# Performance work log

Hardware: AMD Instinct MI355X
Metric: run time of the kernel (lower is better)

The kernel has to match this reference:

```python
import jax, jax.numpy as jnp
import numpy as np
import math

B, S, E, H = 2, 2048, 1024, 16
D = E // H  # head_size = 64
EPS = 1e-5

def _ln(x, g, b):
    mu = jnp.mean(x, axis=-1, keepdims=True)
    var = jnp.mean(jnp.square(x - mu), axis=-1, keepdims=True)
    return (x - mu) * jax.lax.rsqrt(var + EPS) * g + b

def setup_inputs() -> dict:
    key = jax.random.key(0)
    ks = jax.random.split(key, 16)
    s = 0.02
    return {
        "I": jax.random.normal(ks[0], (B, S, E), jnp.float32),
        "x": jax.random.normal(ks[1], (B, S, E), jnp.float32),
        "mask": jnp.ones((B, 1, S), jnp.int32),
        # per-head Q/K/V weights stacked over heads [H, E, D], biases [H, D]
        "wq": jax.random.normal(ks[2], (H, E, D), jnp.float32) * s,
        "bq": jax.random.normal(ks[3], (H, D), jnp.float32) * s,
        "wk": jax.random.normal(ks[4], (H, E, D), jnp.float32) * s,
        "bk": jax.random.normal(ks[5], (H, D), jnp.float32) * s,
        "wv": jax.random.normal(ks[6], (H, E, D), jnp.float32) * s,
        "bv": jax.random.normal(ks[7], (H, D), jnp.float32) * s,
        "w_proj": jax.random.normal(ks[8], (E, E), jnp.float32) * s,
        "b_proj": jnp.zeros((E,), jnp.float32),
        "g1": jnp.ones((E,), jnp.float32),
        "be1": jnp.zeros((E,), jnp.float32),
        "g2": jnp.ones((E,), jnp.float32),
        "be2": jnp.zeros((E,), jnp.float32),
        "w1": jax.random.normal(ks[9], (E, 4 * E), jnp.float32) * s,
        "b1": jnp.zeros((4 * E,), jnp.float32),
        "w2": jax.random.normal(ks[10], (4 * E, E), jnp.float32) * s,
        "b2": jnp.zeros((E,), jnp.float32),
    }

def reference(I, x, mask, wq, bq, wk, bk, wv, bv, w_proj, b_proj,
              g1, be1, g2, be2, w1, b1, w2, b2):
    xn = _ln(x, g1, be1)
    # batched per-head projections: [B,S,E] x [H,E,D] -> [B,H,S,D]
    q = jnp.einsum('bse,hed->bhsd', I, wq) + bq[None, :, None, :]
    k = jnp.einsum('bse,hed->bhsd', xn, wk) + bk[None, :, None, :]
    v = jnp.einsum('bse,hed->bhsd', xn, wv) + bv[None, :, None, :]
    # NOTE: original scales by sqrt(n_embed), not sqrt(head_size)
    scores = jnp.einsum('bhqd,bhkd->bhqk', q, k) / math.sqrt(E)
    scores = jnp.where(mask[:, None, :, :] == 0, -1e9, scores)
    attn = jax.nn.softmax(scores, axis=-1)
    ctx = jnp.einsum('bhqk,bhkd->bhqd', attn, v)
    # concat heads: [B,S,H,D] -> [B,S,E]
    ctx = ctx.transpose(0, 2, 1, 3).reshape(B, S, E)
    attn_out = ctx @ w_proj + b_proj
    h = xn + attn_out
    h2 = _ln(h, g2, be2)
    ff = jax.nn.gelu(h2 @ w1 + b1, approximate=False) @ w2 + b2
    return h2 + ff
```

## Files before the change

kernel.cpp:

```cpp
#include <hip/hip_runtime.h>
#include <hip/hip_bf16.h>
#include <math.h>

typedef short short8 __attribute__((ext_vector_type(8)));
typedef short short4_t __attribute__((ext_vector_type(4)));
typedef float f32x4 __attribute__((ext_vector_type(4)));
typedef unsigned short u16;
typedef unsigned int u32;

#define B_ 2
#define S_ 2048
#define E_ 1024
#define H_ 16
#define D_ 64
#define TOK (B_*S_)

__device__ __forceinline__ float bf2f(u16 u) {
    union { unsigned int u; float f; } v; v.u = ((unsigned int)u) << 16; return v.f;
}
__device__ __forceinline__ u16 f2bf(float f) {
    union { float f; unsigned int u; } v; v.f = f;
    unsigned int r = v.u + 0x7fffu + ((v.u >> 16) & 1u);
    return (u16)(r >> 16);
}
__device__ __forceinline__ u32 fbits(float f) {
    union { float f; u32 u; } v; v.f = f; return v.u;
}
__device__ __forceinline__ void gl_lds16(const u16* g, short* l) {
    __builtin_amdgcn_global_load_lds(
        (const __attribute__((address_space(1))) unsigned int*)(g),
        (__attribute__((address_space(3))) unsigned int*)(l), 16, 0, 0);
}


__device__ __forceinline__ void convf_body(const float* __restrict__ s, u16* __restrict__ d,
                                           int blk, int tid)
{
    size_t i = ((size_t)blk * 256 + tid) * 8;
    f32x4 a = *(const f32x4*)(s + i);
    f32x4 b = *(const f32x4*)(s + i + 4);
    short8 r;
#pragma unroll
    for (int j = 0; j < 4; j++) { r[j] = (short)f2bf(a[j]); r[4 + j] = (short)f2bf(b[j]); }
    *(short8*)(d + i) = r;
}

__device__ __forceinline__ void tconv_body(const float* __restrict__ src, u16* __restrict__ dst,
                                           int K, int N, int bx, int by, u16 (*t)[72], int tid)
{
    int k0 = by * 64, n0 = bx * 64;
    int kr = tid >> 4, nc = (tid & 15) * 4;
#pragma unroll
    for (int i = 0; i < 4; i++) {
        f32x4 v = *(const f32x4*)(src + (size_t)(k0 + kr + i * 16) * N + n0 + nc);
#pragma unroll
        for (int j = 0; j < 4; j++) t[kr + i * 16][nc + j] = f2bf(v[j]);
    }
    __syncthreads();
    int nr = tid >> 2, kg = (tid & 3) * 16;
    short8 r0, r1;
#pragma unroll
    for (int j = 0; j < 8; j++) { r0[j] = (short)t[kg + j][nr]; r1[j] = (short)t[kg + 8 + j][nr]; }
    u16* dp = dst + (size_t)(n0 + nr) * K + k0 + kg;
    *(short8*)(dp) = r0;
    *(short8*)(dp + 8) = r1;
}

__device__ __forceinline__ void tconvqkv_body(const float* __restrict__ wq, const float* __restrict__ wk,
                                              const float* __restrict__ wv, u16* __restrict__ dst,
                                              int z, int yy, u16 (*t)[72], int tid)
{
    int w = z >> 4, hh = z & 15;
    const float* src = (w == 0 ? wq : (w == 1 ? wk : wv)) + (size_t)hh * E_ * D_;
    u16* d = dst + (size_t)w * E_ * E_ + (size_t)hh * D_ * E_;
    int k0 = yy * 64;
    int kr = tid >> 4, nc = (tid & 15) * 4;
#pragma unroll
    for (int i = 0; i < 4; i++) {
        f32x4 v = *(const f32x4*)(src + (size_t)(k0 + kr + i * 16) * D_ + nc);
#pragma unroll
        for (int j = 0; j < 4; j++) t[kr + i * 16][nc + j] = f2bf(v[j]);
    }
    __syncthreads();
    int nr = tid >> 2, kg = (tid & 3) * 16;
    short8 r0, r1;
#pragma unroll
    for (int j = 0; j < 8; j++) { r0[j] = (short)t[kg + j][nr]; r1[j] = (short)t[kg + 8 + j][nr]; }
    u16* dp = d + (size_t)nr * E_ + k0 + kg;
    *(short8*)(dp) = r0;
    *(short8*)(dp + 8) = r1;
}

__device__ __forceinline__ void maskprep_body(const int* __restrict__ mask, float* __restrict__ fb,
                                              int* __restrict__ ok, int b, int tid, unsigned char* fl)
{
    int base = tid * 8;
    unsigned all = 1;
#pragma unroll
    for (int j = 0; j < 8; j++) {
        int m = mask[b * S_ + base + j];
        fb[b * S_ + base + j] = m ? 0.f : -1e9f;
        all &= (m != 0) ? 1u : 0u;
    }
    fl[tid] = (unsigned char)all;
    __syncthreads();
    if (tid < 32) {
        unsigned a = 1;
#pragma unroll
        for (int j = 0; j < 8; j++) a &= fl[tid * 8 + j];
        ok[b * 32 + tid] = (int)a;
    }
}

template<int INF32>
__device__ __forceinline__ void ln_body(const void* __restrict__ xv, const float* __restrict__ g,
                                        const float* __restrict__ be, u16* __restrict__ y,
                                        int blk, int tid)
{
    int lane = tid & 63, wave = tid >> 6;
    int row = blk * 4 + wave;
    int c0 = lane * 16;
    float v[16];
    if (INF32) {
        const float* xr = (const float*)xv + (size_t)row * E_ + c0;
#pragma unroll
        for (int i = 0; i < 4; i++) {
            f32x4 xx = *(const f32x4*)(xr + i * 4);
#pragma unroll
            for (int j = 0; j < 4; j++) v[i * 4 + j] = xx[j];
        }
    } else {
        const u16* xr = (const u16*)xv + (size_t)row * E_ + c0;
        short8 a = *(const short8*)(xr);
        short8 b = *(const short8*)(xr + 8);
#pragma unroll
        for (int j = 0; j < 8; j++) { v[j] = bf2f((u16)a[j]); v[8 + j] = bf2f((u16)b[j]); }
    }
    float s = 0.f, q = 0.f;
#pragma unroll
    for (int i = 0; i < 16; i++) { s += v[i]; q += v[i] * v[i]; }
#pragma unroll
    for (int off = 1; off < 64; off <<= 1) {
        s += __shfl_xor(s, off, 64);
        q += __shfl_xor(q, off, 64);
    }
    float mu = s * (1.0f / E_);
    float var = q * (1.0f / E_) - mu * mu;
    float rstd = rsqrtf(var + 1e-5f);
    u16* yr = y + (size_t)row * E_ + c0;
    short8 o0, o1;
#pragma unroll
    for (int j = 0; j < 8; j++) {
        o0[j] = (short)f2bf((v[j] - mu) * rstd * g[c0 + j] + be[c0 + j]);
        o1[j] = (short)f2bf((v[8 + j] - mu) * rstd * g[c0 + 8 + j] + be[c0 + 8 + j]);
    }
    *(short8*)(yr) = o0;
    *(short8*)(yr + 8) = o1;
}

__global__ __launch_bounds__(256) void prep_k(
    const float* __restrict__ I, u16* __restrict__ Ibf,
    const float* __restrict__ wq, const float* __restrict__ wk,
    const float* __restrict__ wv, u16* __restrict__ WTqkv,
    const float* __restrict__ w_proj, u16* __restrict__ WTproj,
    const float* __restrict__ w1, u16* __restrict__ WT1,
    const float* __restrict__ w2, u16* __restrict__ WT2,
    const int* __restrict__ mask, float* __restrict__ fbm, int* __restrict__ okm,
    const float* __restrict__ x, const float* __restrict__ g1,
    const float* __restrict__ be1, u16* __restrict__ xn)
{
    __shared__ __align__(16) u16 tsh[64][72];
    int id = blockIdx.x, tid = threadIdx.x;
    if (id < 1024) {
        ln_body<1>(x, g1, be1, xn, id, tid);
    } else if (id < 3072) {
        convf_body(I, Ibf, id - 1024, tid);
    } else if (id < 3840) {
        int vb = id - 3072;
        tconvqkv_body(wq, wk, wv, WTqkv, vb >> 4, vb & 15, tsh, tid);
    } else if (id < 4096) {
        int vb = id - 3840;
        tconv_body(w_proj, WTproj, E_, E_, vb & 15, vb >> 4, tsh, tid);
    } else if (id < 5120) {
        int vb = id - 4096;
        tconv_body(w1, WT1, E_, 4 * E_, vb & 63, vb >> 6, tsh, tid);
    } else if (id < 6144) {
        int vb = id - 5120;
        tconv_body(w2, WT2, 4 * E_, E_, vb & 15, vb >> 4, tsh, tid);
    } else {
        maskprep_body(mask, fbm, okm, id - 6144, tid, (unsigned char*)tsh);
    }
}

__global__ __launch_bounds__(256) void vtrans_k(const u16* __restrict__ V, u16* __restrict__ Vt)
{
    __shared__ u16 t[64][72];
    int s0 = blockIdx.x * 64, h = blockIdx.y, b = blockIdx.z;
    int tid = threadIdx.x;
    int sr = tid >> 2, dc = (tid & 3) * 16;
    const u16* src = V + (size_t)b * S_ * E_ + (size_t)(s0 + sr) * E_ + h * D_ + dc;
    short8 v0 = *(const short8*)(src);
    short8 v1 = *(const short8*)(src + 8);
#pragma unroll
    for (int j = 0; j < 8; j++) { t[sr][dc + j] = v0[j]; t[sr][dc + 8 + j] = v1[j]; }
    __syncthreads();
    int dr = tid >> 2, sc = (tid & 3) * 16;
    short8 r0, r1;
#pragma unroll
    for (int j = 0; j < 8; j++) { r0[j] = (short)t[sc + j][dr]; r1[j] = (short)t[sc + 8 + j][dr]; }
    u16* dp = Vt + ((size_t)(b * H_ + h) * D_ + dr) * S_ + s0 + sc;
    *(short8*)(dp) = r0;
    *(short8*)(dp + 8) = r1;
}

template<int INF32>
__global__ __launch_bounds__(256) void ln_kernel(
    const void* __restrict__ xv, const float* __restrict__ g,
    const float* __restrict__ be, u16* __restrict__ y)
{
    ln_body<INF32>(xv, g, be, y, blockIdx.x, threadIdx.x);
}

template<int QKV, int GELU, int RX>
__global__ __launch_bounds__(512) void gemm8p_k(
    const u16* __restrict__ A, const u16* __restrict__ Axn,
    const u16* __restrict__ WT,
    const float* __restrict__ bq, const float* __restrict__ bk, const float* __restrict__ bv,
    u16* __restrict__ C, int M, int N, int K)
{
    __shared__ __align__(16) short As[2][256 * 64];
    __shared__ __align__(16) short Bs[2][256 * 64];
    int tid = threadIdx.x;
    int wave = tid >> 6, lane = tid & 63, quad = lane >> 4, l16 = lane & 15;
    int wm = wave >> 2, wn = wave & 3;

    int gx = gridDim.x, gy = gridDim.y;
    int lin = blockIdx.y * gx + blockIdx.x;
    int xcd = lin & 7, w = lin >> 3;
    int rw = gx / RX, rh = gy / (8 / RX);
    int bx = (xcd % RX) * rw + (w % rw);
    int by = (xcd / RX) * rh + (w / rw);
    int n0 = bx * 256, m0 = by * 256;

    int which = QKV ? (n0 >> 10) : 0;
    const u16* Ause = (QKV && which) ? Axn : A;
    const float* bias = QKV ? (which == 0 ? bq : (which == 1 ? bk : bv)) : bq;

    f32x4 acc[8][4];
#pragma unroll
    for (int m = 0; m < 8; m++)
#pragma unroll
        for (int n = 0; n < 4; n++)
            acc[m][n] = (f32x4){0.f, 0.f, 0.f, 0.f};

    int srow = lane >> 3, slot = lane & 7;
    const u16* Ag = Ause + (size_t)(m0 + wave * 16 + srow) * K + ((slot ^ srow) << 3);
    const u16* Bg = WT + (size_t)(n0 + wave * 16 + srow) * K + ((slot ^ srow) << 3);
    const size_t r8K = (size_t)8 * K, r128K = (size_t)128 * K, r136K = (size_t)136 * K;
    int wv = wave * 1024;
    int r7 = l16 & 7;
    int soff0 = (quad ^ r7) << 3;
    int soff1 = ((4 + quad) ^ r7) << 3;
    int arow = (wm * 128 + l16) * 64;
    int brow = (wn * 64 + l16) * 64;
    int NT = K >> 6;

#define SB __builtin_amdgcn_sched_barrier(0)
#define GLA2P(P, BUF, H) do { \
    gl_lds16((P) + ((H) ? r128K : (size_t)0), &As[BUF][wv + (H) * 8192]); \
    gl_lds16((P) + ((H) ? r136K : r8K), &As[BUF][wv + (H) * 8192 + 512]); } while (0)
#define GLB2P(P, BUF, H) do { \
    gl_lds16((P) + ((H) ? r128K : (size_t)0), &Bs[BUF][wv + (H) * 8192]); \
    gl_lds16((P) + ((H) ? r136K : r8K), &Bs[BUF][wv + (H) * 8192 + 512]); } while (0)
#define RDA(BUF, Mi, SO) (*(const short8*)(&As[BUF][arow + (Mi) * 1024 + (SO)]))
#define RDB(BUF, Ni, SO) (*(const short8*)(&Bs[BUF][brow + (Ni) * 1024 + (SO)]))
#define MM2(mb, R) do { \
    _Pragma("unroll") \
    for (int n_ = 0; n_ < 4; n_++) { \
        acc[(mb)][n_]     = __builtin_amdgcn_mfma_f32_16x16x32_bf16(R[0], bf[n_][0], acc[(mb)][n_], 0, 0, 0); \
        acc[(mb) + 1][n_] = __builtin_amdgcn_mfma_f32_16x16x32_bf16(R[1], bf[n_][0], acc[(mb) + 1][n_], 0, 0, 0); \
    } \
    _Pragma("unroll") \
    for (int n_ = 0; n_ < 4; n_++) { \
        acc[(mb)][n_]     = __builtin_amdgcn_mfma_f32_16x16x32_bf16(R[2], bf[n_][1], acc[(mb)][n_], 0, 0, 0); \
        acc[(mb) + 1][n_] = __builtin_amdgcn_mfma_f32_16x16x32_bf16(R[3], bf[n_][1], acc[(mb) + 1][n_], 0, 0, 0); \
    } \
} while (0)

#define KTILE(BUF, OBUF, TT, AO, BO) do { \
    SB; __builtin_amdgcn_s_barrier(); \
    short8 bf[4][2], af[4], ag[4]; \
    bf[0][0] = RDB(BUF, 0, soff0); bf[1][0] = RDB(BUF, 1, soff0); \
    bf[2][0] = RDB(BUF, 2, soff0); bf[3][0] = RDB(BUF, 3, soff0); \
    af[0] = RDA(BUF, 0, soff0); af[1] = RDA(BUF, 1, soff0); \
    bf[0][1] = RDB(BUF, 0, soff1); bf[1][1] = RDB(BUF, 1, soff1); \
    bf[2][1] = RDB(BUF, 2, soff1); bf[3][1] = RDB(BUF, 3, soff1); \
    af[2] = RDA(BUF, 0, soff1); af[3] = RDA(BUF, 1, soff1); \
    if ((TT) + 1 < NT) GLA2P((AO), OBUF, 0); \
    __builtin_amdgcn_s_setprio(1); MM2(0, af); __builtin_amdgcn_s_setprio(0); \
    ag[0] = RDA(BUF, 2, soff0); ag[1] = RDA(BUF, 3, soff0); \
    ag[2] = RDA(BUF, 2, soff1); ag[3] = RDA(BUF, 3, soff1); \
    SB; __builtin_amdgcn_s_barrier(); \
    if ((TT) + 1 < NT) GLA2P((AO), OBUF, 1); \
    __builtin_amdgcn_s_setprio(1); MM2(2, ag); __builtin_amdgcn_s_setprio(0); \
    af[0] = RDA(BUF, 4, soff0); af[1] = RDA(BUF, 5, soff0); \
    af[2] = RDA(BUF, 4, soff1); af[3] = RDA(BUF, 5, soff1); \
    SB; __builtin_amdgcn_s_barrier(); \
    if ((TT) + 2 < NT) GLB2P((BO), BUF, 0); \
    __builtin_amdgcn_s_setprio(1); MM2(4, af); __builtin_amdgcn_s_setprio(0); \
    ag[0] = RDA(BUF, 6, soff0); ag[1] = RDA(BUF, 7, soff0); \
    ag[2] = RDA(BUF, 6, soff1); ag[3] = RDA(BUF, 7, soff1); \
    SB; __builtin_amdgcn_s_barrier(); \
    if ((TT) + 2 < NT) GLB2P((BO), BUF, 1); \
    __builtin_amdgcn_s_setprio(1); MM2(6, ag); __builtin_amdgcn_s_setprio(0); \
    if ((TT) + 2 < NT) { asm volatile("s_waitcnt vmcnt(4)" ::: "memory"); } \
    else               { asm volatile("s_waitcnt vmcnt(0)" ::: "memory"); } \
    SB; \
} while (0)

    GLB2P(Bg, 0, 0); GLB2P(Bg, 0, 1);
    GLA2P(Ag, 0, 0); GLA2P(Ag, 0, 1);
    if (NT > 1) {
        GLB2P(Bg + 64, 1, 0); GLB2P(Bg + 64, 1, 1);
        asm volatile("s_waitcnt vmcnt(4)" ::: "memory");
    } else {
        asm volatile("s_waitcnt vmcnt(0)" ::: "memory");
    }

    const u16* A1 = Ag + 64;
    const u16* B2 = Bg + 128;
    for (int t = 0; t < NT; t += 2) {
        KTILE(0, 1, t, A1, B2);
        KTILE(1, 0, t + 1, A1 + 64, B2 + 64);
        A1 += 128; B2 += 128;
    }

    u16* Cw = QKV ? (C + (size_t)which * (size_t)M * 1024) : C;
    int ostride = QKV ? 1024 : N;
#pragma unroll
    for (int m = 0; m < 8; m++) {
#pragma unroll
        for (int n = 0; n < 4; n++) {
            int colg = n0 + wn * 64 + n * 16 + l16;
            int col = QKV ? (colg & 1023) : colg;
            float bb = bias[col];
#pragma unroll
            for (int r = 0; r < 4; r++) {
                int row = m0 + wm * 128 + m * 16 + quad * 4 + r;
                float v = acc[m][n][r] + bb;
                if (QKV && which == 0) v *= 0.03125f;
                if (GELU) v = 0.5f * v * (1.0f + erff(v * 0.70710678118f));
                Cw[(size_t)row * ostride + col] = f2bf(v);
            }
        }
    }
#undef SB
#undef GLA2P
#undef GLB2P
#undef RDA
#undef RDB
#undef MM2
#undef KTILE
}

__global__ __launch_bounds__(256) void gemmsk_k(
    const u16* __restrict__ A, const u16* __restrict__ WT,
    u16* __restrict__ P, int M, int N, int K, int Ks)
{
    __shared__ __align__(16) short a_sh[2][128 * 32];
    __shared__ __align__(16) short b_sh[2][128 * 32];
    int tid = threadIdx.x;
    int wave = tid >> 6, lane = tid & 63, quad = lane >> 4, l16 = lane & 15;
    int wm = wave >> 1, wn = wave & 1;
    int gx = gridDim.x;
    int lin = blockIdx.y * gx + blockIdx.x;
    int xcd = lin & 7, w = lin >> 3;
    int rh = gridDim.y >> 3;
    int bx = w % gx, by = xcd * rh + (w / gx);
    int m0 = by * 128, n0 = bx * 128;
    int koff = blockIdx.z * Ks;

    f32x4 acc[4][4];
#pragma unroll
    for (int mt = 0; mt < 4; mt++)
#pragma unroll
        for (int nt = 0; nt < 4; nt++)
            acc[mt][nt] = (f32x4){0.f, 0.f, 0.f, 0.f};

    int srow = lane >> 2;
    int c = ((lane & 3) ^ ((lane >> 3) & 3)) * 8;
    const u16* Ab = A + (size_t)(m0 + wave * 32 + srow) * K + koff + c;
    const u16* Bb = WT + (size_t)(n0 + wave * 32 + srow) * K + koff + c;
    short* al0 = &a_sh[0][wave * 1024];
    short* al1 = &a_sh[1][wave * 1024];
    short* bl0 = &b_sh[0][wave * 1024];
    short* bl1 = &b_sh[1][wave * 1024];
    int xo = (quad ^ ((l16 >> 1) & 3)) * 8;

    for (int kk = 0; kk < Ks; kk += 64) {
        __syncthreads();
        gl_lds16(Ab + kk, al0);
        gl_lds16(Ab + kk + (size_t)16 * K, al0 + 512);
        gl_lds16(Ab + kk + 32, al1);
        gl_lds16(Ab + kk + (size_t)16 * K + 32, al1 + 512);
        gl_lds16(Bb + kk, bl0);
        gl_lds16(Bb + kk + (size_t)16 * K, bl0 + 512);
        gl_lds16(Bb + kk + 32, bl1);
        gl_lds16(Bb + kk + (size_t)16 * K + 32, bl1 + 512);
        __syncthreads();

#pragma unroll
        for (int h = 0; h < 2; h++) {
            short8 af[4], bf8[4];
#pragma unroll
            for (int mt = 0; mt < 4; mt++)
                af[mt] = *(const short8*)(&a_sh[h][(wm * 64 + mt * 16 + l16) * 32 + xo]);
#pragma unroll
            for (int nt = 0; nt < 4; nt++)
                bf8[nt] = *(const short8*)(&b_sh[h][(wn * 64 + nt * 16 + l16) * 32 + xo]);
#pragma unroll
            for (int mt = 0; mt < 4; mt++)
#pragma unroll
                for (int nt = 0; nt < 4; nt++)
                    acc[mt][nt] = __builtin_amdgcn_mfma_f32_16x16x32_bf16(af[mt], bf8[nt], acc[mt][nt], 0, 0, 0);
        }
    }

    u16* Pz = P + (size_t)blockIdx.z * (size_t)M * N;
#pragma unroll
    for (int mt = 0; mt < 4; mt++) {
#pragma unroll
        for (int nt = 0; nt < 4; nt++) {
            int col = n0 + wn * 64 + nt * 16 + l16;
#pragma unroll
            for (int r = 0; r < 4; r++) {
                int row = m0 + wm * 64 + mt * 16 + quad * 4 + r;
                Pz[(size_t)row * N + col] = f2bf(acc[mt][nt][r]);
            }
        }
    }
}

__global__ __launch_bounds__(256) void combine2_k(
    const u16* __restrict__ P, const float* __restrict__ bias,
    const u16* __restrict__ res, float* __restrict__ out)
{
    const size_t MN = (size_t)TOK * E_;
    size_t i = ((size_t)blockIdx.x * 256 + threadIdx.x) * 8;
    int col = (int)(i & (E_ - 1));
    float v[8];
    f32x4 b0 = *(const f32x4*)(bias + col);
    f32x4 b1 = *(const f32x4*)(bias + col + 4);
    short8 rr = *(const short8*)(res + i);
#pragma unroll
    for (int j = 0; j < 4; j++) { v[j] = b0[j] + bf2f((u16)rr[j]); v[4 + j] = b1[j] + bf2f((u16)rr[4 + j]); }
#pragma unroll
    for (int z = 0; z < 2; z++) {
        short8 p = *(const short8*)(P + z * MN + i);
#pragma unroll
        for (int j = 0; j < 8; j++) v[j] += bf2f((u16)p[j]);
    }
    f32x4 o0, o1;
#pragma unroll
    for (int j = 0; j < 4; j++) { o0[j] = v[j]; o1[j] = v[4 + j]; }
    *(f32x4*)(out + i) = o0;
    *(f32x4*)(out + i + 4) = o1;
}

template<int GELU, int RES, int CF32>
__global__ __launch_bounds__(256) void gemm3_k(
    const u16* __restrict__ A, const u16* __restrict__ WT,
    const float* __restrict__ bias, const u16* __restrict__ res,
    void* __restrict__ Cv, int M, int N, int K)
{
    __shared__ __align__(16) short a_sh[2][128 * 32];
    __shared__ __align__(16) short b_sh[2][64 * 32];
    int tid = threadIdx.x;
    int wave = tid >> 6, lane = tid & 63, quad = lane >> 4, l16 = lane & 15;
    int wm = wave >> 1, wn = wave & 1;
    int m0 = blockIdx.y * 128, n0 = blockIdx.x * 64;

    f32x4 acc[4][2];
#pragma unroll
    for (int mt = 0; mt < 4; mt++)
#pragma unroll
        for (int nt = 0; nt < 2; nt++)
            acc[mt][nt] = (f32x4){0.f, 0.f, 0.f, 0.f};

    int srow = lane >> 2;
    int c = ((lane & 3) ^ ((lane >> 3) & 3)) * 8;
    const u16* Ab = A + (size_t)(m0 + wave * 32 + srow) * K + c;
    const u16* Bb = WT + (size_t)(n0 + wave * 16 + srow) * K + c;
    short* al0 = &a_sh[0][wave * 1024];
    short* al1 = &a_sh[1][wave * 1024];
    short* bl0 = &b_sh[0][wave * 512];
    short* bl1 = &b_sh[1][wave * 512];
    int xo = (quad ^ ((l16 >> 1) & 3)) * 8;

    for (int kk = 0; kk < K; kk += 64) {
        __syncthreads();
        gl_lds16(Ab + kk, al0);
        gl_lds16(Ab + kk + (size_t)16 * K, al0 + 512);
        gl_lds16(Ab + kk + 32, al1);
        gl_lds16(Ab + kk + (size_t)16 * K + 32, al1 + 512);
        gl_lds16(Bb + kk, bl0);
        gl_lds16(Bb + kk + 32, bl1);
        __syncthreads();

#pragma unroll
        for (int h = 0; h < 2; h++) {
            short8 af[4], bf8[2];
#pragma unroll
            for (int mt = 0; mt < 4; mt++)
                af[mt] = *(const short8*)(&a_sh[h][(wm * 64 + mt * 16 + l16) * 32 + xo]);
#pragma unroll
            for (int nt = 0; nt < 2; nt++)
                bf8[nt] = *(const short8*)(&b_sh[h][(wn * 32 + nt * 16 + l16) * 32 + xo]);
#pragma unroll
            for (int mt = 0; mt < 4; mt++)
#pragma unroll
                for (int nt = 0; nt < 2; nt++)
                    acc[mt][nt] = __builtin_amdgcn_mfma_f32_16x16x32_bf16(af[mt], bf8[nt], acc[mt][nt], 0, 0, 0);
        }
    }

#pragma unroll
    for (int mt = 0; mt < 4; mt++) {
#pragma unroll
        for (int nt = 0; nt < 2; nt++) {
            int col = n0 + wn * 32 + nt * 16 + l16;
            float bb = bias[col];
#pragma unroll
            for (int r = 0; r < 4; r++) {
                int row = m0 + wm * 64 + mt * 16 + quad * 4 + r;
                float v = acc[mt][nt][r] + bb;
                if (RES) v += bf2f(res[(size_t)row * N + col]);
                if (GELU) v = 0.5f * v * (1.0f + erff(v * 0.70710678118f));
                if (CF32) ((float*)Cv)[(size_t)row * N + col] = v;
                else ((u16*)Cv)[(size_t)row * N + col] = f2bf(v);
            }
        }
    }
}

__global__ __launch_bounds__(512) void attn_k(
    const u16* __restrict__ Q, const u16* __restrict__ K,
    const u16* __restrict__ Vt, const float* __restrict__ fb,
    const int* __restrict__ ok, u16* __restrict__ O)
{
    __shared__ __align__(16) short k_sh[2][2][64 * 32];
    __shared__ __align__(16) short v_sh[2][2][64 * 32];
    __shared__ __align__(16) short p_sh[8][16 * 72];
    int tid = threadIdx.x;
    int wave = tid >> 6, lane = tid & 63, quad = lane >> 4, l16 = lane & 15;
    int lin = blockIdx.x + 16 * (blockIdx.y + 16 * blockIdx.z);
    int xcd = lin & 7, w = lin >> 3;
    int combo = xcd * 4 + (w >> 4);
    int qb = w & 15, h = combo & 15, b = combo >> 4;
    int q0 = qb * 128;
    const u16* Qp = Q + (size_t)b * S_ * E_ + (size_t)h * D_;
    const u16* Kp = K + (size_t)b * S_ * E_ + (size_t)h * D_;
    const u16* Vtp = Vt + (size_t)(b * H_ + h) * D_ * S_;

    int qrow = q0 + wave * 16 + l16;
    short8 qf0 = *(const short8*)(Qp + (size_t)qrow * E_ + quad * 8);
    short8 qf1 = *(const short8*)(Qp + (size_t)qrow * E_ + 32 + quad * 8);

    f32x4 o[4];
#pragma unroll
    for (int dt = 0; dt < 4; dt++) o[dt] = (f32x4){0.f, 0.f, 0.f, 0.f};
    float rs_tot = 0.f;

    int sub = wave & 1, rblk = wave >> 1;
    int srow = lane >> 2;
    int c = ((lane & 3) ^ ((lane >> 3) & 3)) * 8;
    const u16* Kg = Kp + (size_t)(rblk * 16 + srow) * E_ + sub * 32 + c;
    const u16* Vg = Vtp + (size_t)(rblk * 16 + srow) * S_ + sub * 32 + c;
    short* kl0 = &k_sh[0][sub][rblk * 512];
    short* kl1 = &k_sh[1][sub][rblk * 512];
    short* vl0 = &v_sh[0][sub][rblk * 512];
    short* vl1 = &v_sh[1][sub][rblk * 512];

    gl_lds16(Kg, kl0);
    gl_lds16(Vg, vl0);
    __syncthreads();

    const float* fbb = fb + b * S_;
    const int* okb = ok + b * 32;
    int xo = (quad ^ ((l16 >> 1) & 3)) * 8;

    for (int kt = 0; kt < S_ / 64; kt++) {
        int cur = kt & 1;
        if (kt < 31) {
            gl_lds16(Kg + (size_t)(kt + 1) * 64 * E_, cur ? kl0 : kl1);
            gl_lds16(Vg + (kt + 1) * 64, cur ? vl0 : vl1);
        }

        f32x4 s[4];
#pragma unroll
        for (int mt = 0; mt < 4; mt++) {
            int ro = (mt * 16 + l16) * 32 + xo;
            short8 kf0 = *(const short8*)(&k_sh[cur][0][ro]);
            short8 kf1 = *(const short8*)(&k_sh[cur][1][ro]);
            s[mt] = __builtin_amdgcn_mfma_f32_16x16x32_bf16(kf0, qf0, (f32x4){0.f,0.f,0.f,0.f}, 0, 0, 0);
            s[mt] = __builtin_amdgcn_mfma_f32_16x16x32_bf16(kf1, qf1, s[mt], 0, 0, 0);
        }

        if (!okb[kt]) {
#pragma unroll
            for (int mt = 0; mt < 4; mt++)
#pragma unroll
                for (int r = 0; r < 4; r++)
                    s[mt][r] += fbb[kt * 64 + mt * 16 + quad * 4 + r];
        }

#pragma unroll
        for (int mt = 0; mt < 4; mt++) {
            float p0 = __expf(s[mt][0]);
            float p1 = __expf(s[mt][1]);
            float p2 = __expf(s[mt][2]);
            float p3 = __expf(s[mt][3]);
            rs_tot += (p0 + p1) + (p2 + p3);
            u32 u0 = __builtin_amdgcn_perm(fbits(p1), fbits(p0), 0x07060302u);
            u32 u1 = __builtin_amdgcn_perm(fbits(p3), fbits(p2), 0x07060302u);
            uint2 pk; pk.x = u0; pk.y = u1;
            *(uint2*)(&p_sh[wave][l16 * 72 + mt * 16 + quad * 4]) = pk;
        }

#pragma unroll
        for (int sk = 0; sk < 2; sk++) {
            short8 pf = *(const short8*)(&p_sh[wave][l16 * 72 + sk * 32 + quad * 8]);
#pragma unroll
            for (int dt = 0; dt < 4; dt++) {
                short8 vf = *(const short8*)(&v_sh[cur][sk][(dt * 16 + l16) * 32 + xo]);
                o[dt] = __builtin_amdgcn_mfma_f32_16x16x32_bf16(vf, pf, o[dt], 0, 0, 0);
            }
        }
        __syncthreads();
    }

    rs_tot += __shfl_xor(rs_tot, 16, 64);
    rs_tot += __shfl_xor(rs_tot, 32, 64);
    float inv = 1.0f / rs_tot;
    u16* Op = O + (size_t)b * S_ * E_ + (size_t)(q0 + wave * 16 + l16) * E_ + h * D_;
#pragma unroll
    for (int dt = 0; dt < 4; dt++) {
        short4_t pk;
#pragma unroll
        for (int r = 0; r < 4; r++) pk[r] = (short)f2bf(o[dt][r] * inv);
        *(short4_t*)(Op + dt * 16 + quad * 4) = pk;
    }
}

extern "C" void kernel_launch(void* const* d_in, const int* in_sizes, int n_in,
                              void* d_out, int out_size, void* d_ws, size_t ws_size,
                              hipStream_t stream)
{
    (void)in_sizes; (void)n_in; (void)out_size; (void)ws_size;
    const float* I      = (const float*)d_in[0];
    const float* x      = (const float*)d_in[1];
    const int*   mask   = (const int*)d_in[2];
    const float* wq     = (const float*)d_in[3];
    const float* bq     = (const float*)d_in[4];
    const float* wk     = (const float*)d_in[5];
    const float* bk     = (const float*)d_in[6];
    const float* wv     = (const float*)d_in[7];
    const float* bv     = (const float*)d_in[8];
    const float* w_proj = (const float*)d_in[9];
    const float* b_proj = (const float*)d_in[10];
    const float* g1     = (const float*)d_in[11];
    const float* be1    = (const float*)d_in[12];
    const float* g2     = (const float*)d_in[13];
    const float* be2    = (const float*)d_in[14];
    const float* w1     = (const float*)d_in[15];
    const float* b1     = (const float*)d_in[16];
    const float* w2     = (const float*)d_in[17];
    const float* b2     = (const float*)d_in[18];
    float* out = (float*)d_out;

    char* ws = (char*)d_ws;
    const size_t SZ = (size_t)TOK * E_;
    u16* xn   = (u16*)(ws);
    u16* qb_  = (u16*)(ws + SZ * 2);
    u16* kb_  = (u16*)(ws + SZ * 4);
    u16* vb_  = (u16*)(ws + SZ * 6);
    u16* Vt   = (u16*)(ws + SZ * 8);
    u16* Ibf  = (u16*)(ws + SZ * 8);
    u16* ctx  = (u16*)(ws + SZ * 6);
    u16* hb   = (u16*)(ws + SZ * 4);
    u16* h2   = (u16*)(ws);
    u16* a1   = (u16*)(ws + SZ * 2);
    u16* WTqkv  = (u16*)(ws + 40u * 1024 * 1024);
    u16* WTproj = (u16*)(ws + 46u * 1024 * 1024);
    u16* WT1    = (u16*)(ws + 48u * 1024 * 1024);
    u16* WT2    = (u16*)(ws + 56u * 1024 * 1024);
    u16* Pp     = (u16*)(ws + 40u * 1024 * 1024);
    float* fbm  = (float*)(ws + 40u * 1024 * 1024);
    int*   okm  = (int*)(ws + 40u * 1024 * 1024 + 16384);

    prep_k<<<dim3(6146), 256, 0, stream>>>(
        I, Ibf, wq, wk, wv, WTqkv, w_proj, WTproj, w1, WT1, w2, WT2,
        mask, fbm, okm, x, g1, be1, xn);

    gemm8p_k<1,0,2><<<dim3(12, TOK / 256), 512, 0, stream>>>(
        Ibf, xn, WTqkv, bq, bk, bv, qb_, TOK, 3072, E_);

    vtrans_k<<<dim3(S_ / 64, H_, B_), 256, 0, stream>>>(vb_, Vt);

    attn_k<<<dim3(S_ / 128, H_, B_), 512, 0, stream>>>(qb_, kb_, Vt, fbm, okm, ctx);

    gemm3_k<0,1,0><<<dim3(16, TOK / 128), 256, 0, stream>>>(
        ctx, WTproj, b_proj, xn, hb, TOK, E_, E_);
    ln_kernel<0><<<TOK / 4, 256, 0, stream>>>(hb, g2, be2, h2);
    gemm8p_k<0,1,2><<<dim3(16, TOK / 256), 512, 0, stream>>>(
        h2, nullptr, WT1, b1, nullptr, nullptr, a1, TOK, 4 * E_, E_);
    gemmsk_k<<<dim3(8, TOK / 128, 2), 256, 0, stream>>>(
        a1, WT2, Pp, TOK, E_, 4 * E_, 2 * E_);
    combine2_k<<<dim3(TOK * E_ / (256 * 8)), 256, 0, stream>>>(Pp, b2, h2, out);
}
```

Measured before the change: 361.0 us.

## Replace 256x256 K64 ping-pong GEMM with 128x256 K32 multi-block GEMM

Rewrites the QKV and FFN1 GEMM kernel to use 128x256 output tiles with a K-step of 32 and a much smaller LDS footprint. The launch bounds now request 4 blocks per CU so occupancy can hide latency, replacing the hand-scheduled ping-pong pipeline with its setprio and partial waitcnts. The grid doubles in the M direction, giving more blocks for better CU fill. The cost is less data reuse per tile, one full vmcnt(0) wait plus a barrier every K-step, and tighter register limits.

Measured after the change: 357.2 us. No clear change (-1.0%).

```diff
diff --git a/kernel.cpp b/kernel.cpp
--- a/kernel.cpp
+++ b/kernel.cpp
@@ -222,14 +222,14 @@
 }
 
 template<int QKV, int GELU, int RX>
-__global__ __launch_bounds__(512) void gemm8p_k(
+__global__ __launch_bounds__(512, 4) void gemmb32_k(
     const u16* __restrict__ A, const u16* __restrict__ Axn,
     const u16* __restrict__ WT,
     const float* __restrict__ bq, const float* __restrict__ bk, const float* __restrict__ bv,
     u16* __restrict__ C, int M, int N, int K)
 {
-    __shared__ __align__(16) short As[2][256 * 64];
-    __shared__ __align__(16) short Bs[2][256 * 64];
+    __shared__ __align__(16) short As[2][128 * 32];
+    __shared__ __align__(16) short Bs[2][256 * 32];
     int tid = threadIdx.x;
     int wave = tid >> 6, lane = tid & 63, quad = lane >> 4, l16 = lane & 15;
     int wm = wave >> 2, wn = wave & 3;
@@ -240,127 +240,81 @@
     int rw = gx / RX, rh = gy / (8 / RX);
     int bx = (xcd % RX) * rw + (w % rw);
     int by = (xcd / RX) * rh + (w / rw);
-    int n0 = bx * 256, m0 = by * 256;
+    int n0 = bx * 256, m0 = by * 128;
 
     int which = QKV ? (n0 >> 10) : 0;
     const u16* Ause = (QKV && which) ? Axn : A;
     const float* bias = QKV ? (which == 0 ? bq : (which == 1 ? bk : bv)) : bq;
 
-    f32x4 acc[8][4];
-#pragma unroll
-    for (int m = 0; m < 8; m++)
-#pragma unroll
-        for (int n = 0; n < 4; n++)
-            acc[m][n] = (f32x4){0.f, 0.f, 0.f, 0.f};
-
-    int srow = lane >> 3, slot = lane & 7;
-    const u16* Ag = Ause + (size_t)(m0 + wave * 16 + srow) * K + ((slot ^ srow) << 3);
-    const u16* Bg = WT + (size_t)(n0 + wave * 16 + srow) * K + ((slot ^ srow) << 3);
-    const size_t r8K = (size_t)8 * K, r128K = (size_t)128 * K, r136K = (size_t)136 * K;
-    int wv = wave * 1024;
-    int r7 = l16 & 7;
-    int soff0 = (quad ^ r7) << 3;
-    int soff1 = ((4 + quad) ^ r7) << 3;
-    int arow = (wm * 128 + l16) * 64;
-    int brow = (wn * 64 + l16) * 64;
-    int NT = K >> 6;
-
-#define SB __builtin_amdgcn_sched_barrier(0)
-#define GLA2P(P, BUF, H) do { \
-    gl_lds16((P) + ((H) ? r128K : (size_t)0), &As[BUF][wv + (H) * 8192]); \
-    gl_lds16((P) + ((H) ? r136K : r8K), &As[BUF][wv + (H) * 8192 + 512]); } while (0)
-#define GLB2P(P, BUF, H) do { \
-    gl_lds16((P) + ((H) ? r128K : (size_t)0), &Bs[BUF][wv + (H) * 8192]); \
-    gl_lds16((P) + ((H) ? r136K : r8K), &Bs[BUF][wv + (H) * 8192 + 512]); } while (0)
-#define RDA(BUF, Mi, SO) (*(const short8*)(&As[BUF][arow + (Mi) * 1024 + (SO)]))
-#define RDB(BUF, Ni, SO) (*(const short8*)(&Bs[BUF][brow + (Ni) * 1024 + (SO)]))
-#define MM2(mb, R) do { \
-    _Pragma("unroll") \
-    for (int n_ = 0; n_ < 4; n_++) { \
-        acc[(mb)][n_]     = __builtin_amdgcn_mfma_f32_16x16x32_bf16(R[0], bf[n_][0], acc[(mb)][n_], 0, 0, 0); \
-        acc[(mb) + 1][n_] = __builtin_amdgcn_mfma_f32_16x16x32_bf16(R[1], bf[n_][0], acc[(mb) + 1][n_], 0, 0, 0); \
-    } \
-    _Pragma("unroll") \
-    for (int n_ = 0; n_ < 4; n_++) { \
-        acc[(mb)][n_]     = __builtin_amdgcn_mfma_f32_16x16x32_bf16(R[2], bf[n_][1], acc[(mb)][n_], 0, 0, 0); \
-        acc[(mb) + 1][n_] = __builtin_amdgcn_mfma_f32_16x16x32_bf16(R[3], bf[n_][1], acc[(mb) + 1][n_], 0, 0, 0); \
-    } \
-} while (0)
-
-#define KTILE(BUF, OBUF, TT, AO, BO) do { \
-    SB; __builtin_amdgcn_s_barrier(); \
-    short8 bf[4][2], af[4], ag[4]; \
-    bf[0][0] = RDB(BUF, 0, soff0); bf[1][0] = RDB(BUF, 1, soff0); \
-    bf[2][0] = RDB(BUF, 2, soff0); bf[3][0] = RDB(BUF, 3, soff0); \
-    af[0] = RDA(BUF, 0, soff0); af[1] = RDA(BUF, 1, soff0); \
-    bf[0][1] = RDB(BUF, 0, soff1); bf[1][1] = RDB(BUF, 1, soff1); \
-    bf[2][1] = RDB(BUF, 2, soff1); bf[3][1] = RDB(BUF, 3, soff1); \
-    af[2] = RDA(BUF, 0, soff1); af[3] = RDA(BUF, 1, soff1); \
-    if ((TT) + 1 < NT) GLA2P((AO), OBUF, 0); \
-    __builtin_amdgcn_s_setprio(1); MM2(0, af); __builtin_amdgcn_s_setprio(0); \
-    ag[0] = RDA(BUF, 2, soff0); ag[1] = RDA(BUF, 3, soff0); \
-    ag[2] = RDA(BUF, 2, soff1); ag[3] = RDA(BUF, 3, soff1); \
-    SB; __builtin_amdgcn_s_barrier(); \
-    if ((TT) + 1 < NT) GLA2P((AO), OBUF, 1); \
-    __builtin_amdgcn_s_setprio(1); MM2(2, ag); __builtin_amdgcn_s_setprio(0); \
-    af[0] = RDA(BUF, 4, soff0); af[1] = RDA(BUF, 5, soff0); \
-    af[2] = RDA(BUF, 4, soff1); af[3] = RDA(BUF, 5, soff1); \
-    SB; __builtin_amdgcn_s_barrier(); \
-    if ((TT) + 2 < NT) GLB2P((BO), BUF, 0); \
-    __builtin_amdgcn_s_setprio(1); MM2(4, af); __builtin_amdgcn_s_setprio(0); \
-    ag[0] = RDA(BUF, 6, soff0); ag[1] = RDA(BUF, 7, soff0); \
-    ag[2] = RDA(BUF, 6, soff1); ag[3] = RDA(BUF, 7, soff1); \
-    SB; __builtin_amdgcn_s_barrier(); \
-    if ((TT) + 2 < NT) GLB2P((BO), BUF, 1); \
-    __builtin_amdgcn_s_setprio(1); MM2(6, ag); __builtin_amdgcn_s_setprio(0); \
-    if ((TT) + 2 < NT) { asm volatile("s_waitcnt vmcnt(4)" ::: "memory"); } \
-    else               { asm volatile("s_waitcnt vmcnt(0)" ::: "memory"); } \
-    SB; \
-} while (0)
-
-    GLB2P(Bg, 0, 0); GLB2P(Bg, 0, 1);
-    GLA2P(Ag, 0, 0); GLA2P(Ag, 0, 1);
-    if (NT > 1) {
-        GLB2P(Bg + 64, 1, 0); GLB2P(Bg + 64, 1, 1);
-        asm volatile("s_waitcnt vmcnt(4)" ::: "memory");
-    } else {
-        asm volatile("s_waitcnt vmcnt(0)" ::: "memory");
-    }
-
-    const u16* A1 = Ag + 64;
-    const u16* B2 = Bg + 128;
+    f32x4 acc[4][4];
+#pragma unroll
+    for (int mi = 0; mi < 4; mi++)
+#pragma unroll
+        for (int ni = 0; ni < 4; ni++)
+            acc[mi][ni] = (f32x4){0.f, 0.f, 0.f, 0.f};
+
+    int srow = lane >> 2, slot = lane & 3;
+    int kap = (srow >> 1) & 3;
+    const u16* Ag = Ause + (size_t)(m0 + wave * 16 + srow) * K + ((slot ^ kap) << 3);
+    const u16* Bg = WT + (size_t)(n0 + wave * 32 + srow) * K + ((slot ^ kap) << 3);
+    const size_t r16K = (size_t)16 * K;
+    int wA = wave * 512, wB = wave * 1024;
+    int so = (quad ^ ((l16 >> 1) & 3)) << 3;
+    int aoff = (wm * 64 + l16) * 32 + so;
+    int boff = (wn * 64 + l16) * 32 + so;
+    int NT = K >> 5;
+
+#define STAGEK(BUF, PA, PB) do { \
+    gl_lds16((PA), &As[BUF][wA]); \
+    gl_lds16((PB), &Bs[BUF][wB]); \
+    gl_lds16((PB) + r16K, &Bs[BUF][wB + 512]); } while (0)
+
+#define TILEK(BUF, OBUF, TT, PA, PB) do { \
+    if ((TT) + 1 < NT) STAGEK(OBUF, (PA), (PB)); \
+    short8 af[4], bf[4]; \
+    const short* ab = &As[BUF][aoff]; \
+    const short* bb = &Bs[BUF][boff]; \
+    _Pragma("unroll") for (int i_ = 0; i_ < 4; i_++) af[i_] = *(const short8*)(ab + i_ * 512); \
+    _Pragma("unroll") for (int i_ = 0; i_ < 4; i_++) bf[i_] = *(const short8*)(bb + i_ * 512); \
+    _Pragma("unroll") for (int mi = 0; mi < 4; mi++) \
+    _Pragma("unroll") for (int ni = 0; ni < 4; ni++) \
+        acc[mi][ni] = __builtin_amdgcn_mfma_f32_16x16x32_bf16(af[mi], bf[ni], acc[mi][ni], 0, 0, 0); \
+    asm volatile("s_waitcnt vmcnt(0)" ::: "memory"); \
+    __builtin_amdgcn_s_barrier(); } while (0)
+
+    STAGEK(0, Ag, Bg);
+    asm volatile("s_waitcnt vmcnt(0)" ::: "memory");
+    __builtin_amdgcn_s_barrier();
+
+    const u16* PA = Ag + 32;
+    const u16* PB = Bg + 32;
     for (int t = 0; t < NT; t += 2) {
-        KTILE(0, 1, t, A1, B2);
-        KTILE(1, 0, t + 1, A1 + 64, B2 + 64);
-        A1 += 128; B2 += 128;
+        TILEK(0, 1, t, PA, PB);
+        TILEK(1, 0, t + 1, PA + 32, PB + 32);
+        PA += 64; PB += 64;
     }
 
     u16* Cw = QKV ? (C + (size_t)which * (size_t)M * 1024) : C;
     int ostride = QKV ? 1024 : N;
 #pragma unroll
-    for (int m = 0; m < 8; m++) {
-#pragma unroll
-        for (int n = 0; n < 4; n++) {
-            int colg = n0 + wn * 64 + n * 16 + l16;
+    for (int mi = 0; mi < 4; mi++) {
+#pragma unroll
+        for (int ni = 0; ni < 4; ni++) {
+            int colg = n0 + wn * 64 + ni * 16 + l16;
             int col = QKV ? (colg & 1023) : colg;
             float bb = bias[col];
 #pragma unroll
             for (int r = 0; r < 4; r++) {
-                int row = m0 + wm * 128 + m * 16 + quad * 4 + r;
-                float v = acc[m][n][r] + bb;
+                int row = m0 + wm * 64 + mi * 16 + quad * 4 + r;
+                float v = acc[mi][ni][r] + bb;
                 if (QKV && which == 0) v *= 0.03125f;
                 if (GELU) v = 0.5f * v * (1.0f + erff(v * 0.70710678118f));
                 Cw[(size_t)row * ostride + col] = f2bf(v);
             }
         }
     }
-#undef SB
-#undef GLA2P
-#undef GLB2P
-#undef RDA
-#undef RDB
-#undef MM2
-#undef KTILE
+#undef STAGEK
+#undef TILEK
 }
 
 __global__ __launch_bounds__(256) void gemmsk_k(
@@ -702,7 +656,7 @@
         I, Ibf, wq, wk, wv, WTqkv, w_proj, WTproj, w1, WT1, w2, WT2,
         mask, fbm, okm, x, g1, be1, xn);
 
-    gemm8p_k<1,0,2><<<dim3(12, TOK / 256), 512, 0, stream>>>(
+    gemmb32_k<1,0,2><<<dim3(12, TOK / 128), 512, 0, stream>>>(
         Ibf, xn, WTqkv, bq, bk, bv, qb_, TOK, 3072, E_);
 
     vtrans_k<<<dim3(S_ / 64, H_, B_), 256, 0, stream>>>(vb_, Vt);
@@ -712,7 +666,7 @@
     gemm3_k<0,1,0><<<dim3(16, TOK / 128), 256, 0, stream>>>(
         ctx, WTproj, b_proj, xn, hb, TOK, E_, E_);
     ln_kernel<0><<<TOK / 4, 256, 0, stream>>>(hb, g2, be2, h2);
-    gemm8p_k<0,1,2><<<dim3(16, TOK / 256), 512, 0, stream>>>(
+    gemmb32_k<0,1,2><<<dim3(16, TOK / 128), 512, 0, stream>>>(
         h2, nullptr, WT1, b1, nullptr, nullptr, a1, TOK, 4 * E_, E_);
     gemmsk_k<<<dim3(8, TOK / 128, 2), 256, 0, stream>>>(
         a1, WT2, Pp, TOK, E_, 4 * E_, 2 * E_);
```
